# Kernel optimization log

Measured on AMD Instinct MI355X. Metric: run time of the kernel, lower is better.

Reference implementation:

```python
import jax, jax.numpy as jnp
import numpy as np

N_NODES = 50000

def gcn_conv(x, W, b, row, col, ew, n):
    # PyG GCNConv: linear first (no bias in lin), then gcn_norm with added
    # self-loops (weight 1.0), symmetric D^{-1/2} normalization, scatter-add
    # aggregation from row (source) to col (target), then bias.
    h = x @ W                                      # [N, out]
    loop = jnp.arange(n, dtype=row.dtype)
    row_f = jnp.concatenate([row, loop])
    col_f = jnp.concatenate([col, loop])
    ew_f = jnp.concatenate([ew, jnp.ones((n,), dtype=ew.dtype)])
    deg = jax.ops.segment_sum(ew_f, col_f, num_segments=n)
    dinv = jnp.where(deg > 0, jax.lax.rsqrt(jnp.maximum(deg, 1e-30)), 0.0)
    norm = dinv[row_f] * ew_f * dinv[col_f]        # [E+N]
    msg = norm[:, None] * h[row_f]                 # gather + scale
    out = jax.ops.segment_sum(msg, col_f, num_segments=n)  # scatter-add
    return out + b

def setup_inputs() -> dict:
    key = jax.random.key(0)
    k = jax.random.split(key, 8)
    in_dim, hidden_dim, out_dim = 128, 256, 128
    n, e = N_NODES, 600000
    x = jax.random.normal(k[0], (n, in_dim), dtype=jnp.float32)
    edge_index = jax.random.randint(k[1], (2, e), 0, n, dtype=jnp.int64)
    edge_weight = jax.random.uniform(k[2], (e,), dtype=jnp.float32)
    # Glorot-style params (PyG GCNConv lin has no bias; bias added after aggregation)
    W1 = jax.random.normal(k[3], (in_dim, hidden_dim), dtype=jnp.float32) / np.sqrt(in_dim)
    b1 = jnp.zeros((hidden_dim,), dtype=jnp.float32)
    W2 = jax.random.normal(k[4], (hidden_dim, out_dim), dtype=jnp.float32) / np.sqrt(hidden_dim)
    b2 = jnp.zeros((out_dim,), dtype=jnp.float32)
    return {"x": x, "edge_index": edge_index, "edge_weight": edge_weight,
            "W1": W1, "b1": b1, "W2": W2, "b2": b2}

def reference(x, edge_index, edge_weight, W1, b1, W2, b2):
    n = x.shape[0]
    row, col = edge_index[0], edge_index[1]
    h = jax.nn.relu(gcn_conv(x, W1, b1, row, col, edge_weight, n))
    # dropout is identity in eval mode
    out = jax.nn.relu(gcn_conv(h, W2, b2, row, col, edge_weight, n))
    return out
```

## Files before the change

kernel.cpp:

```cpp
#include <hip/hip_runtime.h>
#include <hip/hip_bf16.h>

constexpr int IN_DIM  = 128;
constexpr int HID     = 256;
constexpr int OUT_DIM = 128;
constexpr int ELL_W   = 64;

typedef __attribute__((ext_vector_type(8))) short short8;
typedef __attribute__((ext_vector_type(8))) unsigned short ushort8;
typedef __attribute__((ext_vector_type(4))) float f32x4;

__device__ __forceinline__ float bf2f(unsigned short u) {
    return __uint_as_float(((unsigned int)u) << 16);
}
__device__ __forceinline__ unsigned short f2bf(float f) {
    unsigned int u = __float_as_uint(f);
    u += 0x7FFFu + ((u >> 16) & 1u);
    return (unsigned short)(u >> 16);
}
__device__ __forceinline__ unsigned short f2h(float f) {
    _Float16 h = (_Float16)f;
    unsigned short b;
    __builtin_memcpy(&b, &h, 2);
    return b;
}
__device__ __forceinline__ float h2f(unsigned short b) {
    _Float16 h;
    __builtin_memcpy(&h, &b, 2);
    return (float)h;
}
__device__ __forceinline__ unsigned int pack_e(int src, float w) {
    return (unsigned int)src | ((unsigned int)f2h(w) << 16);
}

__device__ __forceinline__ void ell_gather_acc(
    const unsigned int* __restrict__ bucket, int m,
    const unsigned short* __restrict__ tab, int j8, int gw, int l16,
    float acc[8]) {
    for (int base = 0; base < m; base += 16) {
        const unsigned int mt = (base + l16 < m) ? bucket[base + l16] : 0u;
        const int c16   = min(m - base, 16);
        const int quads = (c16 + 3) >> 2;
        unsigned int u[4];
        ushort8 v[4];
        #pragma unroll
        for (int i = 0; i < 4; ++i) {
            u[i] = __shfl(mt, gw * 16 + i);
            v[i] = *(const ushort8*)&tab[(size_t)(u[i] & 0xFFFFu) * 128 + j8];
        }
        for (int q = 1; q < quads; ++q) {
            unsigned int nu[4];
            ushort8 nv[4];
            #pragma unroll
            for (int i = 0; i < 4; ++i) {
                nu[i] = __shfl(mt, gw * 16 + q * 4 + i);
                nv[i] = *(const ushort8*)&tab[(size_t)(nu[i] & 0xFFFFu) * 128 + j8];
            }
            #pragma unroll
            for (int i = 0; i < 4; ++i) {
                const float f = h2f((unsigned short)(u[i] >> 16));
                #pragma unroll
                for (int k = 0; k < 8; ++k) acc[k] = fmaf(f, bf2f(v[i][k]), acc[k]);
            }
            #pragma unroll
            for (int i = 0; i < 4; ++i) { u[i] = nu[i]; v[i] = nv[i]; }
        }
        #pragma unroll
        for (int i = 0; i < 4; ++i) {
            const float f = h2f((unsigned short)(u[i] >> 16));
            #pragma unroll
            for (int k = 0; k < 8; ++k) acc[k] = fmaf(f, bf2f(v[i][k]), acc[k]);
        }
    }
}

__global__ void k_prep(int* __restrict__ cnt, int n,
                       const float* __restrict__ W1, unsigned short* __restrict__ w1t,
                       const float* __restrict__ W2, unsigned short* __restrict__ w2t) {
    const int i = blockIdx.x * 256 + threadIdx.x;
    if (i < n) cnt[i] = 0;
    if (i < IN_DIM * HID) {
        const int k = i / HID, nn = i % HID;
        w1t[(size_t)nn * IN_DIM + k] = f2bf(W1[i]);
    }
    if (i < HID * OUT_DIM) {
        const int k = i / OUT_DIM, nn = i % OUT_DIM;
        w2t[(size_t)nn * HID + k] = f2bf(W2[i]);
    }
}

__global__ void k_fill_ell(const int* __restrict__ row, const int* __restrict__ col,
                           const float* __restrict__ ew, int* __restrict__ cnt,
                           unsigned int* __restrict__ ell, int E) {
    const int i  = blockIdx.x * blockDim.x + threadIdx.x;
    const int e0 = i * 4;
    if (e0 + 3 < E) {
        const int4   c4 = *reinterpret_cast<const int4*>(col + e0);
        const int4   r4 = *reinterpret_cast<const int4*>(row + e0);
        const float4 w4 = *reinterpret_cast<const float4*>(ew + e0);
        const int p0 = atomicAdd(&cnt[c4.x], 1);
        const int p1 = atomicAdd(&cnt[c4.y], 1);
        const int p2 = atomicAdd(&cnt[c4.z], 1);
        const int p3 = atomicAdd(&cnt[c4.w], 1);
        if (p0 < ELL_W) ell[(size_t)c4.x * ELL_W + p0] = pack_e(r4.x, w4.x);
        if (p1 < ELL_W) ell[(size_t)c4.y * ELL_W + p1] = pack_e(r4.y, w4.y);
        if (p2 < ELL_W) ell[(size_t)c4.z * ELL_W + p2] = pack_e(r4.z, w4.z);
        if (p3 < ELL_W) ell[(size_t)c4.w * ELL_W + p3] = pack_e(r4.w, w4.w);
    } else {
        for (int e = e0; e < E; ++e) {
            const int c = col[e];
            const int p = atomicAdd(&cnt[c], 1);
            if (p < ELL_W) ell[(size_t)c * ELL_W + p] = pack_e(row[e], ew[e]);
        }
    }
}

__global__ __launch_bounds__(256)
void k_deg_xs(const int* __restrict__ cnt, const unsigned int* __restrict__ ell,
              const float* __restrict__ x, float* __restrict__ dinv,
              unsigned short* __restrict__ xs, int n) {
    const int wave = threadIdx.x >> 6;
    const int lane = threadIdx.x & 63;
    const int node = blockIdx.x * 4 + wave;
    if (node >= n) return;
    const int m = min(cnt[node], ELL_W);
    float s = (lane < m) ? h2f((unsigned short)(ell[(size_t)node * ELL_W + lane] >> 16)) : 0.f;
    #pragma unroll
    for (int d = 32; d; d >>= 1) s += __shfl_xor(s, d);
    const float di = rsqrtf(1.0f + s);
    if (lane == 0) dinv[node] = di;
    const float2 v = *reinterpret_cast<const float2*>(x + (size_t)node * IN_DIM + lane * 2);
    const unsigned int packed = (unsigned int)f2bf(v.x * di) |
                                ((unsigned int)f2bf(v.y * di) << 16);
    *reinterpret_cast<unsigned int*>(xs + (size_t)node * IN_DIM + lane * 2) = packed;
}

template<bool BIAS_RELU, bool BF16OUT>
__global__ __launch_bounds__(256)
void k_gather_w(const int* __restrict__ cnt, const unsigned int* __restrict__ ell,
                const float* __restrict__ dinv, const unsigned short* __restrict__ hs,
                const float* __restrict__ bias, void* __restrict__ out_, int n) {
    constexpr int F = 128;
    const int gid  = threadIdx.x >> 4;
    const int gw   = gid & 3;
    const int l16  = threadIdx.x & 15;
    const int j8   = l16 * 8;
    const int node = blockIdx.x * 16 + gid;
    if (node >= n) return;

    const int m = min(cnt[node], ELL_W);
    const unsigned int* bucket = ell + (size_t)node * ELL_W;

    const float dc = dinv[node];
    const ushort8 hv = *reinterpret_cast<const ushort8*>(hs + (size_t)node * F + j8);

    float acc[8] = {};
    ell_gather_acc(bucket, m, hs, j8, gw, l16, acc);

    float o[8];
    if (BIAS_RELU) {
        const float4 b0 = *reinterpret_cast<const float4*>(bias + j8);
        const float4 b1 = *reinterpret_cast<const float4*>(bias + j8 + 4);
        const float bb[8] = {b0.x, b0.y, b0.z, b0.w, b1.x, b1.y, b1.z, b1.w};
        #pragma unroll
        for (int i = 0; i < 8; ++i)
            o[i] = fmaxf(fmaf(dc, acc[i] + bf2f(hv[i]), bb[i]), 0.f);
    } else {
        #pragma unroll
        for (int i = 0; i < 8; ++i) o[i] = dc * (acc[i] + bf2f(hv[i]));
    }
    if (BF16OUT) {
        unsigned short ob[8];
        #pragma unroll
        for (int i = 0; i < 8; ++i) ob[i] = f2bf(o[i]);
        *reinterpret_cast<uint4*>((unsigned short*)out_ + (size_t)node * F + j8) =
            *reinterpret_cast<uint4*>(ob);
    } else {
        float* op = (float*)out_ + (size_t)node * F + j8;
        *reinterpret_cast<float4*>(op)     = make_float4(o[0], o[1], o[2], o[3]);
        *reinterpret_cast<float4*>(op + 4) = make_float4(o[4], o[5], o[6], o[7]);
    }
}

__global__ __launch_bounds__(256)
void k_gemm1(const unsigned short* __restrict__ A,
             const unsigned short* __restrict__ W1t,
             const float* __restrict__ b1,
             unsigned short* __restrict__ H1,
             int ntiles) {
    __shared__ unsigned short As[2][32 * 128];
    __shared__ unsigned short Hs[32 * 256];

    const int t    = threadIdx.x;
    const int w    = t >> 6;
    const int lane = t & 63;
    const int quad = lane >> 4;
    const int l16  = lane & 15;
    const int xr   = (l16 & 7) << 3;

    short8 bw[4][4];
    #pragma unroll
    for (int nt = 0; nt < 4; ++nt)
        #pragma unroll
        for (int ks = 0; ks < 4; ++ks)
            bw[nt][ks] = *(const short8*)&W1t[(size_t)(w * 64 + nt * 16 + l16) * 128 + ks * 32 + quad * 8];
    float bv[4];
    #pragma unroll
    for (int nt = 0; nt < 4; ++nt) bv[nt] = b1[w * 64 + nt * 16 + l16];

    auto stage = [&](int buf, int tile) {
        #pragma unroll
        for (int j = 0; j < 2; ++j) {
            const int ci = j * 256 + t;
            const int r  = ci >> 4;
            const int c  = (ci & 15) ^ (r & 7);
            __builtin_amdgcn_global_load_lds(
                (const __attribute__((address_space(1))) uint32_t*)(A + ((size_t)tile * 32 + r) * 128 + c * 8),
                (__attribute__((address_space(3))) uint32_t*)(&As[buf][ci * 8]), 16, 0, 0);
        }
    };
    auto mma = [&](int buf, f32x4 (&acc)[2][4]) {
        #pragma unroll
        for (int ks = 0; ks < 4; ++ks) {
            short8 af[2];
            #pragma unroll
            for (int mt = 0; mt < 2; ++mt)
                af[mt] = *(const short8*)&As[buf][(mt * 16 + l16) * 128 + ((ks * 32 + quad * 8) ^ xr)];
            #pragma unroll
            for (int mt = 0; mt < 2; ++mt)
                #pragma unroll
                for (int nt = 0; nt < 4; ++nt)
                    acc[mt][nt] = __builtin_amdgcn_mfma_f32_16x16x32_bf16(
                        af[mt], bw[nt][ks], acc[mt][nt], 0, 0, 0);
        }
    };
    auto epi_store = [&](f32x4 (&acc)[2][4]) {
        #pragma unroll
        for (int mt = 0; mt < 2; ++mt)
            #pragma unroll
            for (int i = 0; i < 4; ++i) {
                const int r  = mt * 16 + quad * 4 + i;
                const int xw = (r & 7) << 3;
                #pragma unroll
                for (int nt = 0; nt < 4; ++nt) {
                    const int col = w * 64 + nt * 16 + l16;
                    Hs[r * 256 + (col ^ xw)] = f2bf(fmaxf(acc[mt][nt][i] + bv[nt], 0.f));
                }
            }
    };
    auto copy_out = [&](int tile) {
        #pragma unroll
        for (int j = 0; j < 4; ++j) {
            const int ci = j * 256 + t;
            const int r  = ci >> 5;
            const int cr = ci & 31;
            *(uint4*)&H1[((size_t)tile * 32 + r) * 256 + cr * 8] =
                *(const uint4*)&Hs[r * 256 + ((cr ^ (r & 7)) * 8)];
        }
    };

    const int t0 = blockIdx.x;
    const int t1 = blockIdx.x + gridDim.x;

    stage(0, t0);
    __syncthreads();
    if (t1 < ntiles) stage(1, t1);
    {
        f32x4 acc[2][4] = {};
        mma(0, acc);
        epi_store(acc);
    }
    __syncthreads();
    copy_out(t0);
    if (t1 < ntiles) {
        f32x4 acc[2][4] = {};
        mma(1, acc);
        __syncthreads();
        epi_store(acc);
        __syncthreads();
        copy_out(t1);
    }
}

__global__ __launch_bounds__(256)
void k_gemm2(const unsigned short* __restrict__ H1,
             const unsigned short* __restrict__ W2t,
             const float* __restrict__ dinv,
             unsigned short* __restrict__ H2,
             int n, int ntiles) {
    __shared__ unsigned short As[2][32 * 256];
    __shared__ unsigned short Hs[32 * 128];

    const int t    = threadIdx.x;
    const int w    = t >> 6;
    const int lane = t & 63;
    const int quad = lane >> 4;
    const int l16  = lane & 15;
    const int xr   = (l16 & 7) << 3;

    short8 bw[2][8];
    #pragma unroll
    for (int nt = 0; nt < 2; ++nt)
        #pragma unroll
        for (int ks = 0; ks < 8; ++ks)
            bw[nt][ks] = *(const short8*)&W2t[(size_t)(w * 32 + nt * 16 + l16) * 256 + ks * 32 + quad * 8];

    auto stage = [&](int buf, int tile) {
        #pragma unroll
        for (int j = 0; j < 4; ++j) {
            const int ci = j * 256 + t;
            const int r  = ci >> 5;
            const int c  = (ci & 31) ^ (r & 7);
            __builtin_amdgcn_global_load_lds(
                (const __attribute__((address_space(1))) uint32_t*)(H1 + ((size_t)tile * 32 + r) * 256 + c * 8),
                (__attribute__((address_space(3))) uint32_t*)(&As[buf][ci * 8]), 16, 0, 0);
        }
    };
    auto mma = [&](int buf, f32x4 (&acc)[2][2]) {
        #pragma unroll
        for (int ks = 0; ks < 8; ++ks) {
            short8 af[2];
            #pragma unroll
            for (int mt = 0; mt < 2; ++mt)
                af[mt] = *(const short8*)&As[buf][(mt * 16 + l16) * 256 + ((ks * 32 + quad * 8) ^ xr)];
            #pragma unroll
            for (int mt = 0; mt < 2; ++mt)
                #pragma unroll
                for (int nt = 0; nt < 2; ++nt)
                    acc[mt][nt] = __builtin_amdgcn_mfma_f32_16x16x32_bf16(
                        af[mt], bw[nt][ks], acc[mt][nt], 0, 0, 0);
        }
    };
    auto epi_store = [&](f32x4 (&acc)[2][2], int tile) {
        #pragma unroll
        for (int mt = 0; mt < 2; ++mt)
            #pragma unroll
            for (int i = 0; i < 4; ++i) {
                const int r  = mt * 16 + quad * 4 + i;
                const int rg = tile * 32 + r;
                const float dr = (rg < n) ? dinv[rg] : 0.f;
                const int xw = (r & 7) << 3;
                #pragma unroll
                for (int nt = 0; nt < 2; ++nt) {
                    const int col = w * 32 + nt * 16 + l16;
                    Hs[r * 128 + (col ^ xw)] = f2bf(acc[mt][nt][i] * dr);
                }
            }
    };
    auto copy_out = [&](int tile) {
        #pragma unroll
        for (int j = 0; j < 2; ++j) {
            const int ci = j * 256 + t;
            const int r  = ci >> 4;
            const int cr = ci & 15;
            *(uint4*)&H2[((size_t)tile * 32 + r) * 128 + cr * 8] =
                *(const uint4*)&Hs[r * 128 + ((cr ^ (r & 7)) * 8)];
        }
    };

    const int t0 = blockIdx.x;
    const int t1 = blockIdx.x + gridDim.x;

    stage(0, t0);
    __syncthreads();
    if (t1 < ntiles) stage(1, t1);
    {
        f32x4 acc[2][2] = {};
        mma(0, acc);
        epi_store(acc, t0);
    }
    __syncthreads();
    copy_out(t0);
    if (t1 < ntiles) {
        f32x4 acc[2][2] = {};
        mma(1, acc);
        __syncthreads();
        epi_store(acc, t1);
        __syncthreads();
        copy_out(t1);
    }
}

extern "C" void kernel_launch(void* const* d_in, const int* in_sizes, int n_in,
                              void* d_out, int out_size, void* d_ws, size_t ws_size,
                              hipStream_t stream) {
    const float* x  = (const float*)d_in[0];
    const int*   ei = (const int*)d_in[1];
    const float* ew = (const float*)d_in[2];
    const float* W1 = (const float*)d_in[3];
    const float* b1 = (const float*)d_in[4];
    const float* W2 = (const float*)d_in[5];
    const float* b2 = (const float*)d_in[6];
    float* out = (float*)d_out;

    const int n = in_sizes[0] / IN_DIM;
    const int E = in_sizes[1] / 2;
    const int Mpad = (n + 127) & ~127;
    const int ntiles = Mpad / 32;
    const int* row = ei;
    const int* col = ei + E;

    float* ws = (float*)d_ws;
    size_t o = 0;
    auto alloc = [&](size_t words) { float* p = ws + o; o += (words + 63) & ~(size_t)63; return p; };
    float* dinv = alloc(n);
    int*   cnt  = (int*)alloc(n);
    unsigned int* ell = (unsigned int*)alloc((size_t)n * ELL_W);
    unsigned short* xs   = (unsigned short*)alloc((size_t)Mpad * IN_DIM / 2);
    unsigned short* aggx = (unsigned short*)alloc((size_t)Mpad * IN_DIM / 2);
    unsigned short* h1   = (unsigned short*)alloc((size_t)Mpad * HID / 2);
    unsigned short* h2s  = (unsigned short*)alloc((size_t)Mpad * OUT_DIM / 2);
    unsigned short* w1t  = (unsigned short*)alloc((size_t)IN_DIM * HID / 2);
    unsigned short* w2t  = (unsigned short*)alloc((size_t)HID * OUT_DIM / 2);

    k_prep<<<(n + 255) / 256, 256, 0, stream>>>(cnt, n, W1, w1t, W2, w2t);
    k_fill_ell<<<(E / 4 + 255) / 256, 256, 0, stream>>>(row, col, ew, cnt, ell, E);
    k_deg_xs<<<(n + 3) / 4, 256, 0, stream>>>(cnt, ell, x, dinv, xs, n);

    k_gather_w<false, true><<<(n + 15) / 16, 256, 0, stream>>>(cnt, ell, dinv, xs, nullptr, aggx, n);

    k_gemm1<<<ntiles / 2, 256, 0, stream>>>(aggx, w1t, b1, h1, ntiles);
    k_gemm2<<<ntiles / 2, 256, 0, stream>>>(h1, w2t, dinv, h2s, n, ntiles);

    k_gather_w<true, false><<<(n + 15) / 16, 256, 0, stream>>>(cnt, ell, dinv, h2s, b2, out, n);
}
```

Before: 207.6 us.

## Fuse the two GEMMs into one kernel keeping the hidden tile in LDS

```diff
diff --git a/kernel.cpp b/kernel.cpp
--- a/kernel.cpp
+++ b/kernel.cpp
@@ -102,15 +102,15 @@
         const int p1 = atomicAdd(&cnt[c4.y], 1);
         const int p2 = atomicAdd(&cnt[c4.z], 1);
         const int p3 = atomicAdd(&cnt[c4.w], 1);
-        if (p0 < ELL_W) ell[(size_t)c4.x * ELL_W + p0] = pack_e(r4.x, w4.x);
-        if (p1 < ELL_W) ell[(size_t)c4.y * ELL_W + p1] = pack_e(r4.y, w4.y);
-        if (p2 < ELL_W) ell[(size_t)c4.z * ELL_W + p2] = pack_e(r4.z, w4.z);
-        if (p3 < ELL_W) ell[(size_t)c4.w * ELL_W + p3] = pack_e(r4.w, w4.w);
+        if (p0 < ELL_W) __builtin_nontemporal_store(pack_e(r4.x, w4.x), &ell[(size_t)c4.x * ELL_W + p0]);
+        if (p1 < ELL_W) __builtin_nontemporal_store(pack_e(r4.y, w4.y), &ell[(size_t)c4.y * ELL_W + p1]);
+        if (p2 < ELL_W) __builtin_nontemporal_store(pack_e(r4.z, w4.z), &ell[(size_t)c4.z * ELL_W + p2]);
+        if (p3 < ELL_W) __builtin_nontemporal_store(pack_e(r4.w, w4.w), &ell[(size_t)c4.w * ELL_W + p3]);
     } else {
         for (int e = e0; e < E; ++e) {
             const int c = col[e];
             const int p = atomicAdd(&cnt[c], 1);
-            if (p < ELL_W) ell[(size_t)c * ELL_W + p] = pack_e(row[e], ew[e]);
+            if (p < ELL_W) __builtin_nontemporal_store(pack_e(row[e], ew[e]), &ell[(size_t)c * ELL_W + p]);
         }
     }
 }
@@ -182,14 +182,17 @@
     }
 }
 
-__global__ __launch_bounds__(256)
-void k_gemm1(const unsigned short* __restrict__ A,
-             const unsigned short* __restrict__ W1t,
-             const float* __restrict__ b1,
-             unsigned short* __restrict__ H1,
-             int ntiles) {
+__global__ __launch_bounds__(256, 2)
+void k_gemm_fused(const unsigned short* __restrict__ A,
+                  const unsigned short* __restrict__ W1t,
+                  const unsigned short* __restrict__ W2t,
+                  const float* __restrict__ b1,
+                  const float* __restrict__ dinv,
+                  unsigned short* __restrict__ H2,
+                  int n, int tpb) {
     __shared__ unsigned short As[2][32 * 128];
     __shared__ unsigned short Hs[32 * 256];
+    __shared__ unsigned short Os[32 * 128];
 
     const int t    = threadIdx.x;
     const int w    = t >> 6;
@@ -198,15 +201,23 @@
     const int l16  = lane & 15;
     const int xr   = (l16 & 7) << 3;
 
-    short8 bw[4][4];
+    short8 bw1[4][4];
     #pragma unroll
     for (int nt = 0; nt < 4; ++nt)
         #pragma unroll
         for (int ks = 0; ks < 4; ++ks)
-            bw[nt][ks] = *(const short8*)&W1t[(size_t)(w * 64 + nt * 16 + l16) * 128 + ks * 32 + quad * 8];
+            bw1[nt][ks] = *(const short8*)&W1t[(size_t)(w * 64 + nt * 16 + l16) * 128 + ks * 32 + quad * 8];
+    short8 bw2[2][8];
+    #pragma unroll
+    for (int nt = 0; nt < 2; ++nt)
+        #pragma unroll
+        for (int ks = 0; ks < 8; ++ks)
+            bw2[nt][ks] = *(const short8*)&W2t[(size_t)(w * 32 + nt * 16 + l16) * 256 + ks * 32 + quad * 8];
     float bv[4];
     #pragma unroll
     for (int nt = 0; nt < 4; ++nt) bv[nt] = b1[w * 64 + nt * 16 + l16];
+
+    const int tile0 = blockIdx.x * tpb;
 
     auto stage = [&](int buf, int tile) {
         #pragma unroll
@@ -219,22 +230,30 @@
                 (__attribute__((address_space(3))) uint32_t*)(&As[buf][ci * 8]), 16, 0, 0);
         }
     };
-    auto mma = [&](int buf, f32x4 (&acc)[2][4]) {
+
+    stage(0, tile0);
+    __syncthreads();
+
+    for (int it = 0; it < tpb; ++it) {
+        const int tile = tile0 + it;
+        if (it + 1 < tpb) stage((it + 1) & 1, tile + 1);
+
+        f32x4 acc1[2][4] = {};
         #pragma unroll
         for (int ks = 0; ks < 4; ++ks) {
             short8 af[2];
             #pragma unroll
             for (int mt = 0; mt < 2; ++mt)
-                af[mt] = *(const short8*)&As[buf][(mt * 16 + l16) * 128 + ((ks * 32 + quad * 8) ^ xr)];
+                af[mt] = *(const short8*)&As[it & 1][(mt * 16 + l16) * 128 + ((ks * 32 + quad * 8) ^ xr)];
             #pragma unroll
             for (int mt = 0; mt < 2; ++mt)
                 #pragma unroll
                 for (int nt = 0; nt < 4; ++nt)
-                    acc[mt][nt] = __builtin_amdgcn_mfma_f32_16x16x32_bf16(
-                        af[mt], bw[nt][ks], acc[mt][nt], 0, 0, 0);
-        }
-    };
-    auto epi_store = [&](f32x4 (&acc)[2][4]) {
+                    acc1[mt][nt] = __builtin_amdgcn_mfma_f32_16x16x32_bf16(
+                        af[mt], bw1[nt][ks], acc1[mt][nt], 0, 0, 0);
+        }
+        __syncthreads();
+
         #pragma unroll
         for (int mt = 0; mt < 2; ++mt)
             #pragma unroll
@@ -244,94 +263,26 @@
                 #pragma unroll
                 for (int nt = 0; nt < 4; ++nt) {
                     const int col = w * 64 + nt * 16 + l16;
-                    Hs[r * 256 + (col ^ xw)] = f2bf(fmaxf(acc[mt][nt][i] + bv[nt], 0.f));
+                    Hs[r * 256 + (col ^ xw)] = f2bf(fmaxf(acc1[mt][nt][i] + bv[nt], 0.f));
                 }
             }
-    };
-    auto copy_out = [&](int tile) {
-        #pragma unroll
-        for (int j = 0; j < 4; ++j) {
-            const int ci = j * 256 + t;
-            const int r  = ci >> 5;
-            const int cr = ci & 31;
-            *(uint4*)&H1[((size_t)tile * 32 + r) * 256 + cr * 8] =
-                *(const uint4*)&Hs[r * 256 + ((cr ^ (r & 7)) * 8)];
-        }
-    };
-
-    const int t0 = blockIdx.x;
-    const int t1 = blockIdx.x + gridDim.x;
-
-    stage(0, t0);
-    __syncthreads();
-    if (t1 < ntiles) stage(1, t1);
-    {
-        f32x4 acc[2][4] = {};
-        mma(0, acc);
-        epi_store(acc);
-    }
-    __syncthreads();
-    copy_out(t0);
-    if (t1 < ntiles) {
-        f32x4 acc[2][4] = {};
-        mma(1, acc);
         __syncthreads();
-        epi_store(acc);
-        __syncthreads();
-        copy_out(t1);
-    }
-}
-
-__global__ __launch_bounds__(256)
-void k_gemm2(const unsigned short* __restrict__ H1,
-             const unsigned short* __restrict__ W2t,
-             const float* __restrict__ dinv,
-             unsigned short* __restrict__ H2,
-             int n, int ntiles) {
-    __shared__ unsigned short As[2][32 * 256];
-    __shared__ unsigned short Hs[32 * 128];
-
-    const int t    = threadIdx.x;
-    const int w    = t >> 6;
-    const int lane = t & 63;
-    const int quad = lane >> 4;
-    const int l16  = lane & 15;
-    const int xr   = (l16 & 7) << 3;
-
-    short8 bw[2][8];
-    #pragma unroll
-    for (int nt = 0; nt < 2; ++nt)
-        #pragma unroll
-        for (int ks = 0; ks < 8; ++ks)
-            bw[nt][ks] = *(const short8*)&W2t[(size_t)(w * 32 + nt * 16 + l16) * 256 + ks * 32 + quad * 8];
-
-    auto stage = [&](int buf, int tile) {
-        #pragma unroll
-        for (int j = 0; j < 4; ++j) {
-            const int ci = j * 256 + t;
-            const int r  = ci >> 5;
-            const int c  = (ci & 31) ^ (r & 7);
-            __builtin_amdgcn_global_load_lds(
-                (const __attribute__((address_space(1))) uint32_t*)(H1 + ((size_t)tile * 32 + r) * 256 + c * 8),
-                (__attribute__((address_space(3))) uint32_t*)(&As[buf][ci * 8]), 16, 0, 0);
-        }
-    };
-    auto mma = [&](int buf, f32x4 (&acc)[2][2]) {
+
+        f32x4 acc2[2][2] = {};
         #pragma unroll
         for (int ks = 0; ks < 8; ++ks) {
             short8 af[2];
             #pragma unroll
             for (int mt = 0; mt < 2; ++mt)
-                af[mt] = *(const short8*)&As[buf][(mt * 16 + l16) * 256 + ((ks * 32 + quad * 8) ^ xr)];
+                af[mt] = *(const short8*)&Hs[(mt * 16 + l16) * 256 + ((ks * 32 + quad * 8) ^ xr)];
             #pragma unroll
             for (int mt = 0; mt < 2; ++mt)
                 #pragma unroll
                 for (int nt = 0; nt < 2; ++nt)
-                    acc[mt][nt] = __builtin_amdgcn_mfma_f32_16x16x32_bf16(
-                        af[mt], bw[nt][ks], acc[mt][nt], 0, 0, 0);
-        }
-    };
-    auto epi_store = [&](f32x4 (&acc)[2][2], int tile) {
+                    acc2[mt][nt] = __builtin_amdgcn_mfma_f32_16x16x32_bf16(
+                        af[mt], bw2[nt][ks], acc2[mt][nt], 0, 0, 0);
+        }
+
         #pragma unroll
         for (int mt = 0; mt < 2; ++mt)
             #pragma unroll
@@ -343,41 +294,19 @@
                 #pragma unroll
                 for (int nt = 0; nt < 2; ++nt) {
                     const int col = w * 32 + nt * 16 + l16;
-                    Hs[r * 128 + (col ^ xw)] = f2bf(acc[mt][nt][i] * dr);
+                    Os[r * 128 + (col ^ xw)] = f2bf(acc2[mt][nt][i] * dr);
                 }
             }
-    };
-    auto copy_out = [&](int tile) {
+        __syncthreads();
+
         #pragma unroll
         for (int j = 0; j < 2; ++j) {
             const int ci = j * 256 + t;
             const int r  = ci >> 4;
             const int cr = ci & 15;
             *(uint4*)&H2[((size_t)tile * 32 + r) * 128 + cr * 8] =
-                *(const uint4*)&Hs[r * 128 + ((cr ^ (r & 7)) * 8)];
-        }
-    };
-
-    const int t0 = blockIdx.x;
-    const int t1 = blockIdx.x + gridDim.x;
-
-    stage(0, t0);
-    __syncthreads();
-    if (t1 < ntiles) stage(1, t1);
-    {
-        f32x4 acc[2][2] = {};
-        mma(0, acc);
-        epi_store(acc, t0);
-    }
-    __syncthreads();
-    copy_out(t0);
-    if (t1 < ntiles) {
-        f32x4 acc[2][2] = {};
-        mma(1, acc);
-        __syncthreads();
-        epi_store(acc, t1);
-        __syncthreads();
-        copy_out(t1);
+                *(const uint4*)&Os[r * 128 + ((cr ^ (r & 7)) * 8)];
+        }
     }
 }
 
@@ -397,6 +326,7 @@
     const int E = in_sizes[1] / 2;
     const int Mpad = (n + 127) & ~127;
     const int ntiles = Mpad / 32;
+    const int TPB = 4;
     const int* row = ei;
     const int* col = ei + E;
 
@@ -408,7 +338,6 @@
     unsigned int* ell = (unsigned int*)alloc((size_t)n * ELL_W);
     unsigned short* xs   = (unsigned short*)alloc((size_t)Mpad * IN_DIM / 2);
     unsigned short* aggx = (unsigned short*)alloc((size_t)Mpad * IN_DIM / 2);
-    unsigned short* h1   = (unsigned short*)alloc((size_t)Mpad * HID / 2);
     unsigned short* h2s  = (unsigned short*)alloc((size_t)Mpad * OUT_DIM / 2);
     unsigned short* w1t  = (unsigned short*)alloc((size_t)IN_DIM * HID / 2);
     unsigned short* w2t  = (unsigned short*)alloc((size_t)HID * OUT_DIM / 2);
@@ -419,8 +348,7 @@
 
     k_gather_w<false, true><<<(n + 15) / 16, 256, 0, stream>>>(cnt, ell, dinv, xs, nullptr, aggx, n);
 
-    k_gemm1<<<ntiles / 2, 256, 0, stream>>>(aggx, w1t, b1, h1, ntiles);
-    k_gemm2<<<ntiles / 2, 256, 0, stream>>>(h1, w2t, dinv, h2s, n, ntiles);
+    k_gemm_fused<<<ntiles / TPB, 256, 0, stream>>>(aggx, w1t, w2t, b1, dinv, h2s, n, TPB);
 
     k_gather_w<true, false><<<(n + 15) / 16, 256, 0, stream>>>(cnt, ell, dinv, h2s, b2, out, n);
 }
```

New measurement: 204.5 us. No clear change (-1.5%).
